# Kernel optimization log

Measured on AMD Instinct MI355X. Metric: run time of the kernel, lower is better.

Reference implementation:

```python
import jax, jax.numpy as jnp
import numpy as np

jax.config.update("jax_enable_x64", True)  # hash math uses int64, matching torch promotion

NUM_LEVELS = 16
MIN_RES = 16
MAX_RES = 1024
LOG2_T = 19
T = 2 ** LOG2_T          # hash table size per level
FEATS = 2                # features per level
HASH_INIT_SCALE = 0.001
N = 524288               # number of query points

# 8 cube corners; bit==1 selects ceil coordinate (weight = offset), bit==0 selects floor (weight = 1-offset)
CORNER_BITS = np.array([[(b >> 2) & 1, (b >> 1) & 1, b & 1] for b in range(8)], dtype=np.int64)
PRIMES = np.array([1, 2654435761, 805459861], dtype=np.int64)


def setup_inputs() -> dict:
    key = jax.random.key(0)
    k1, k2 = jax.random.split(key)
    x = jax.random.uniform(k1, (N, 3), dtype=jnp.float32, minval=-1.0, maxval=1.0)
    hash_table = (jax.random.uniform(k2, (T * NUM_LEVELS, FEATS), dtype=jnp.float32) * 2.0 - 1.0) * HASH_INIT_SCALE
    return {"x": x, "hash_table": hash_table}


def reference(x, hash_table):
    # per-level resolutions: floor(min_res * growth^level)
    growth = np.exp((np.log(MAX_RES) - np.log(MIN_RES)) / (NUM_LEVELS - 1))
    scalings = jnp.asarray(np.floor(MIN_RES * growth ** np.arange(NUM_LEVELS)), dtype=jnp.float32)  # [L]
    hash_offset = jnp.arange(NUM_LEVELS, dtype=jnp.int64) * T  # [L]

    x01 = x * 0.5 + 0.5                                # map [-1,1] -> [0,1]
    scaled = x01[..., None, :] * scalings[:, None]     # [N, L, 3]
    sc = jnp.ceil(scaled).astype(jnp.int64)            # [N, L, 3]
    sf = jnp.floor(scaled).astype(jnp.int64)           # [N, L, 3]
    offset = scaled - sf.astype(scaled.dtype)          # [N, L, 3] in [0,1)

    bits = jnp.asarray(CORNER_BITS)                    # [8, 3]
    # corner integer coords: [N, L, 8, 3]
    corners = jnp.where(bits[None, None] == 1, sc[:, :, None, :], sf[:, :, None, :])

    # Instant-NGP spatial hash (int64, matching torch's type promotion)
    p = corners * jnp.asarray(PRIMES)
    h = jnp.bitwise_xor(jnp.bitwise_xor(p[..., 0], p[..., 1]), p[..., 2])
    h = h % T + hash_offset[None, :, None]             # [N, L, 8]

    # trilinear weights: prod over dims of (offset if ceil else 1-offset)
    w = jnp.prod(jnp.where(bits[None, None] == 1, offset[:, :, None, :], 1.0 - offset[:, :, None, :]), axis=-1)  # [N, L, 8]

    feats = hash_table[h]                              # [N, L, 8, F] gather
    enc = jnp.sum(feats * w[..., None], axis=-2)       # [N, L, F]
    return enc.reshape(*enc.shape[:-2], NUM_LEVELS * FEATS)  # [N, L*F]
```

## Files before the change

### kernel.cpp

```cpp
#include <hip/hip_runtime.h>
#include <cmath>

#define TBL_SIZE (1u << 19)
#define TBL_MASK (TBL_SIZE - 1u)
#define PRIME1 2654435761u
#define PRIME2 805459861u
#define NUM_LEVELS 16
#define HARD0 6
#define PPB 32

struct ScaleArgs { float s[NUM_LEVELS]; };

typedef float v2f __attribute__((ext_vector_type(2)));

template<int CTRL>
__device__ __forceinline__ float dpp_add(float v) {
    int i = __builtin_bit_cast(int, v);
    int j = __builtin_amdgcn_mov_dpp(i, CTRL, 0xF, 0xF, true);
    return v + __builtin_bit_cast(float, j);
}

__global__ __launch_bounds__(256) void HashEncoding_88837103551034_kernel(
    const float* __restrict__ x,
    const float* __restrict__ table,
    float* __restrict__ out,
    int npoints, int CH, int perXcdHard, int hardTotal, int easyTotal,
    ScaleArgs sc)
{
    int b = blockIdx.x;
    int xcd = b & 7;
    int s = b >> 3;

    int level, chunk;
    if (s < perXcdHard) {
        int g = xcd * perXcdHard + s;
        if (g >= hardTotal) return;
        int li = g / CH;
        level = HARD0 + li;
        chunk = g - li * CH;
    } else {
        int g = (s - perXcdHard) * 8 + xcd;
        if (g >= easyTotal) return;
        int li = g / CH;
        level = li;
        chunk = g - li * CH;
    }

    int t = (int)threadIdx.x;
    int corner = t & 7;
    int n = chunk * PPB + (t >> 3);
    if (n >= npoints) return;

    float x0 = x[(size_t)n * 3 + 0] * 0.5f + 0.5f;
    float x1 = x[(size_t)n * 3 + 1] * 0.5f + 0.5f;
    float x2 = x[(size_t)n * 3 + 2] * 0.5f + 0.5f;

    float sl = sc.s[level];
    float sx = x0 * sl, sy = x1 * sl, sz = x2 * sl;
    float fx = floorf(sx), fy = floorf(sy), fz = floorf(sz);
    float ox = sx - fx, oy = sy - fy, oz = sz - fz;

    int bx = (corner >> 2) & 1, by = (corner >> 1) & 1, bz = corner & 1;

    uint32_t h = (uint32_t)((int)fx + bx)
               ^ ((uint32_t)((int)fy + by) * PRIME1)
               ^ ((uint32_t)((int)fz + bz) * PRIME2);

    const float2* tb = reinterpret_cast<const float2*>(table) + (size_t)level * TBL_SIZE;
    float2 f = tb[h & TBL_MASK];

    float w = (bx ? ox : 1.f - ox)
            * (by ? oy : 1.f - oy)
            * (bz ? oz : 1.f - oz);

    float e0 = f.x * w;
    float e1 = f.y * w;

    e0 = dpp_add<0xB1>(e0);  e1 = dpp_add<0xB1>(e1);
    e0 = dpp_add<0x4E>(e0);  e1 = dpp_add<0x4E>(e1);
    e0 = dpp_add<0x141>(e0); e1 = dpp_add<0x141>(e1);

    if (corner == 0) {
        v2f res; res.x = e0; res.y = e1;
        __builtin_nontemporal_store(res, (v2f*)(out + (size_t)n * (NUM_LEVELS * 2) + level * 2));
    }
}

extern "C" void kernel_launch(void* const* d_in, const int* in_sizes, int n_in,
                              void* d_out, int out_size, void* d_ws, size_t ws_size,
                              hipStream_t stream) {
    const float* x = (const float*)d_in[0];
    const float* table = (const float*)d_in[1];
    float* out = (float*)d_out;
    int npoints = in_sizes[0] / 3;

    ScaleArgs sc;
    double growth = std::exp((std::log(1024.0) - std::log(16.0)) / 15.0);
    for (int l = 0; l < NUM_LEVELS; ++l) {
        sc.s[l] = (float)std::floor(16.0 * std::pow(growth, (double)l));
    }

    int CH = (npoints + PPB - 1) / PPB;
    int nHard = NUM_LEVELS - HARD0;
    int hardTotal = nHard * CH;
    int easyTotal = HARD0 * CH;
    int perXcdHard = (hardTotal + 7) / 8;
    int perXcdEasy = (easyTotal + 7) / 8;
    int grid = 8 * (perXcdHard + perXcdEasy);

    HashEncoding_88837103551034_kernel<<<grid, 256, 0, stream>>>(
        x, table, out, npoints, CH, perXcdHard, hardTotal, easyTotal, sc);
}
```

Baseline: 257.4 us.

## Build dense bf16 grids for coarse levels and bf16-packed hash tables for the rest

Before the main kernel, each call runs preprocessing kernels. These build dense, directly indexed bf16 grids for the coarse levels and convert the remaining hash-table levels into packed bf16 pairs in the workspace. The gather then loads 4 bytes per corner instead of 8. Dense grids also give spatially coherent access on coarse levels, so the random gathers should hit the caches more often. In exchange, every call pays the conversion and build traffic, and features lose precision through bf16 rounding, which risks accuracy-tolerance failures. Work scheduling is also adjusted, with level 6 kept in the hard group when the maximum number of dense levels is built.

After: 272.1 us. 1.06x slower.

```diff
diff --git a/kernel.cpp b/kernel.cpp
--- a/kernel.cpp
+++ b/kernel.cpp
@@ -6,10 +6,14 @@
 #define PRIME1 2654435761u
 #define PRIME2 805459861u
 #define NUM_LEVELS 16
-#define HARD0 6
+#define DLMAX 7
 #define PPB 32
 
-struct ScaleArgs { float s[NUM_LEVELS]; };
+struct Args {
+    float s[NUM_LEVELS];
+    uint32_t doff[DLMAX];
+    int ddim[DLMAX];
+};
 
 typedef float v2f __attribute__((ext_vector_type(2)));
 
@@ -20,69 +24,104 @@
     return v + __builtin_bit_cast(float, j);
 }
 
+__device__ __forceinline__ uint32_t f2bf(float f) {
+    uint32_t u = __builtin_bit_cast(uint32_t, f);
+    return (u + 0x7FFFu + ((u >> 16) & 1u)) >> 16;
+}
+__device__ __forceinline__ float bflo(uint32_t v) { return __builtin_bit_cast(float, v << 16); }
+__device__ __forceinline__ float bfhi(uint32_t v) { return __builtin_bit_cast(float, v & 0xFFFF0000u); }
+
+__global__ __launch_bounds__(256) void cvt_hashed_kernel(
+    const float* __restrict__ table, uint32_t* __restrict__ dst, int DL, int nentries)
+{
+    int gid = blockIdx.x * 256 + (int)threadIdx.x;
+    if (gid >= nentries) return;
+    float2 e = reinterpret_cast<const float2*>(table)[((size_t)DL << 19) + gid];
+    dst[gid] = f2bf(e.x) | (f2bf(e.y) << 16);
+}
+
+__global__ __launch_bounds__(256) void build_dense_kernel(
+    const float* __restrict__ table, uint32_t* __restrict__ dst,
+    uint32_t doff, int dim, int level, int nentries)
+{
+    int id = blockIdx.x * 256 + (int)threadIdx.x;
+    if (id >= nentries) return;
+    int d2 = dim * dim;
+    int xp = id / d2; int rem = id - xp * d2;
+    int yp = rem / dim; int zp = rem - yp * dim;
+    uint32_t h = (uint32_t)xp ^ ((uint32_t)yp * PRIME1) ^ ((uint32_t)zp * PRIME2);
+    float2 e = reinterpret_cast<const float2*>(table)[((size_t)level << 19) + (h & TBL_MASK)];
+    dst[doff + id] = f2bf(e.x) | (f2bf(e.y) << 16);
+}
+
 __global__ __launch_bounds__(256) void HashEncoding_88837103551034_kernel(
     const float* __restrict__ x,
     const float* __restrict__ table,
+    const uint32_t* __restrict__ ws32,
     float* __restrict__ out,
     int npoints, int CH, int perXcdHard, int hardTotal, int easyTotal,
-    ScaleArgs sc)
+    int DL, int NBF, uint32_t bfbase,
+    Args args)
 {
-    int b = blockIdx.x;
-    int xcd = b & 7;
-    int s = b >> 3;
+    int b = blockIdx.x; int xcd = b & 7; int sb = b >> 3;
+    int t = (int)threadIdx.x;
+    int corner = t & 7;
 
     int level, chunk;
-    if (s < perXcdHard) {
-        int g = xcd * perXcdHard + s;
+    if (sb < perXcdHard) {
+        int g = xcd * perXcdHard + sb;
         if (g >= hardTotal) return;
-        int li = g / CH;
-        level = HARD0 + li;
-        chunk = g - li * CH;
+        int li = g / CH; chunk = g - li * CH;
+        if (DL == DLMAX) level = (li == 0) ? 6 : 6 + li;
+        else             level = DL + li;
     } else {
-        int g = (s - perXcdHard) * 8 + xcd;
+        int g = (sb - perXcdHard) * 8 + xcd;
         if (g >= easyTotal) return;
-        int li = g / CH;
+        int li = g / CH; chunk = g - li * CH;
         level = li;
-        chunk = g - li * CH;
     }
 
-    int t = (int)threadIdx.x;
-    int corner = t & 7;
     int n = chunk * PPB + (t >> 3);
     if (n >= npoints) return;
 
     float x0 = x[(size_t)n * 3 + 0] * 0.5f + 0.5f;
     float x1 = x[(size_t)n * 3 + 1] * 0.5f + 0.5f;
     float x2 = x[(size_t)n * 3 + 2] * 0.5f + 0.5f;
-
-    float sl = sc.s[level];
+    float sl = args.s[level];
     float sx = x0 * sl, sy = x1 * sl, sz = x2 * sl;
     float fx = floorf(sx), fy = floorf(sy), fz = floorf(sz);
     float ox = sx - fx, oy = sy - fy, oz = sz - fz;
-
     int bx = (corner >> 2) & 1, by = (corner >> 1) & 1, bz = corner & 1;
 
-    uint32_t h = (uint32_t)((int)fx + bx)
-               ^ ((uint32_t)((int)fy + by) * PRIME1)
-               ^ ((uint32_t)((int)fz + bz) * PRIME2);
+    float f0, f1;
+    if (level < DL) {
+        int dim = args.ddim[level];
+        int idx = (((int)fx + bx) * dim + (int)fy + by) * dim + (int)fz + bz;
+        uint32_t v = ws32[args.doff[level] + idx];
+        f0 = bflo(v); f1 = bfhi(v);
+    } else {
+        uint32_t h = (uint32_t)((int)fx + bx)
+                   ^ ((uint32_t)((int)fy + by) * PRIME1)
+                   ^ ((uint32_t)((int)fz + bz) * PRIME2);
+        uint32_t idx = h & TBL_MASK;
+        int li = level - DL;
+        if (li < NBF) {
+            uint32_t v = ws32[bfbase + ((size_t)li << 19) + idx];
+            f0 = bflo(v); f1 = bfhi(v);
+        } else {
+            float2 f = reinterpret_cast<const float2*>(table)[((size_t)level << 19) + idx];
+            f0 = f.x; f1 = f.y;
+        }
+    }
 
-    const float2* tb = reinterpret_cast<const float2*>(table) + (size_t)level * TBL_SIZE;
-    float2 f = tb[h & TBL_MASK];
-
-    float w = (bx ? ox : 1.f - ox)
-            * (by ? oy : 1.f - oy)
-            * (bz ? oz : 1.f - oz);
-
-    float e0 = f.x * w;
-    float e1 = f.y * w;
-
+    float w = (bx ? ox : 1.f - ox) * (by ? oy : 1.f - oy) * (bz ? oz : 1.f - oz);
+    float e0 = f0 * w, e1 = f1 * w;
     e0 = dpp_add<0xB1>(e0);  e1 = dpp_add<0xB1>(e1);
     e0 = dpp_add<0x4E>(e0);  e1 = dpp_add<0x4E>(e1);
     e0 = dpp_add<0x141>(e0); e1 = dpp_add<0x141>(e1);
-
     if (corner == 0) {
         v2f res; res.x = e0; res.y = e1;
-        __builtin_nontemporal_store(res, (v2f*)(out + (size_t)n * (NUM_LEVELS * 2) + level * 2));
+        __builtin_nontemporal_store(res, (v2f*)(out + (size_t)n * 32 + level * 2));
     }
 }
 
@@ -94,20 +133,49 @@
     float* out = (float*)d_out;
     int npoints = in_sizes[0] / 3;
 
-    ScaleArgs sc;
+    Args args;
     double growth = std::exp((std::log(1024.0) - std::log(16.0)) / 15.0);
-    for (int l = 0; l < NUM_LEVELS; ++l) {
-        sc.s[l] = (float)std::floor(16.0 * std::pow(growth, (double)l));
+    for (int l = 0; l < NUM_LEVELS; ++l)
+        args.s[l] = (float)std::floor(16.0 * std::pow(growth, (double)l));
+    for (int l = 0; l < DLMAX; ++l) { args.doff[l] = 0; args.ddim[l] = 1; }
+
+    uint64_t cum4 = 0; int DL = 0;
+    int nent_d[DLMAX];
+    for (int l = 0; l < DLMAX; ++l) {
+        int dim = (int)args.s[l] + 2;
+        uint64_t ent = (uint64_t)dim * dim * dim;
+        if ((cum4 + ent) * 4 > ws_size) break;
+        args.doff[l] = (uint32_t)cum4; args.ddim[l] = dim;
+        nent_d[l] = (int)ent;
+        cum4 += ent; DL = l + 1;
+    }
+    uint64_t used = cum4 * 4;
+    int NBF = 0; uint32_t bfbase = (uint32_t)cum4;
+    if (ws_size > used) {
+        NBF = (int)((ws_size - used) / ((uint64_t)TBL_SIZE * 4));
+        if (NBF > NUM_LEVELS - DL) NBF = NUM_LEVELS - DL;
+    }
+
+    uint32_t* ws32 = (uint32_t*)d_ws;
+    if (NBF > 0) {
+        int nent = NBF << 19;
+        cvt_hashed_kernel<<<(nent + 255) / 256, 256, 0, stream>>>(table, ws32 + bfbase, DL, nent);
+    }
+    for (int l = 0; l < DL; ++l) {
+        build_dense_kernel<<<(nent_d[l] + 255) / 256, 256, 0, stream>>>(
+            table, ws32, args.doff[l], args.ddim[l], l, nent_d[l]);
     }
 
     int CH = (npoints + PPB - 1) / PPB;
-    int nHard = NUM_LEVELS - HARD0;
-    int hardTotal = nHard * CH;
-    int easyTotal = HARD0 * CH;
+    int elvls = (DL > 6) ? 6 : DL;
+    int hardUnits = (NUM_LEVELS - DL) + (DL == DLMAX ? 1 : 0);
+    int hardTotal = hardUnits * CH;
+    int easyTotal = elvls * CH;
     int perXcdHard = (hardTotal + 7) / 8;
     int perXcdEasy = (easyTotal + 7) / 8;
     int grid = 8 * (perXcdHard + perXcdEasy);
 
     HashEncoding_88837103551034_kernel<<<grid, 256, 0, stream>>>(
-        x, table, out, npoints, CH, perXcdHard, hardTotal, easyTotal, sc);
+        x, table, ws32, out, npoints, CH, perXcdHard, hardTotal, easyTotal,
+        DL, NBF, bfbase, args);
 }
```
